# Kernel tuning notes

Measured on AMD Instinct MI355X. Metric: run time of the kernel, lower is better.

Reference implementation:

```python
import jax, jax.numpy as jnp
import numpy as np

N, L, G = 8192, 120, 256          # sentences, seq_len, bags
V, P = 80000, 202                 # word vocab, position vocab
WDIM, FDIM = 50, 5                # word_size, feature_size (width = 50+2*5 = 60)
D, C = 230, 53                    # cnn_layers, num_classes


def setup_inputs() -> dict:
    key = jax.random.key(0)
    ks = jax.random.split(key, 9)
    x = jax.random.randint(ks[0], (N, L), 0, V, dtype=jnp.int32)
    ldist = jax.random.randint(ks[1], (N, L), 0, P, dtype=jnp.int32)
    rdist = jax.random.randint(ks[2], (N, L), 0, P, dtype=jnp.int32)
    # cumulative bag boundaries: 256 equal bags of 32 sentences
    total_shape = (jnp.arange(G + 1, dtype=jnp.int32) * (N // G))
    Wv = jax.random.normal(ks[3], (V, WDIM), dtype=jnp.float32) * 0.1
    pf1 = jax.random.normal(ks[4], (P, FDIM), dtype=jnp.float32) * 0.1
    pf2 = jax.random.normal(ks[5], (P, FDIM), dtype=jnp.float32) * 0.1
    Wc = jax.random.normal(ks[6], (D, 1, 3, WDIM + 2 * FDIM), dtype=jnp.float32) * 0.05
    bc = jnp.zeros((D,), dtype=jnp.float32)
    Wr = jax.random.normal(ks[7], (C, D), dtype=jnp.float32) * 0.05
    br = jnp.zeros((C,), dtype=jnp.float32)
    return dict(x=x, ldist=ldist, rdist=rdist, total_shape=total_shape,
                Wv=Wv, pf1=pf1, pf2=pf2, Wc=Wc, bc=bc, Wr=Wr, br=br)


def reference(x, ldist, rdist, total_shape, Wv, pf1, pf2, Wc, bc, Wr, br):
    n = x.shape[0]
    g = total_shape.shape[0] - 1
    # getEmbeddings: concat word + two position embeddings -> (N, L, 60)
    emb = jnp.concatenate([Wv[x], pf1[ldist], pf2[rdist]], axis=-1)
    # Conv2d(1, D, (3, 60)), VALID -> (N, D, L-2, 1)
    conv = jax.lax.conv_general_dilated(
        emb[:, None, :, :], Wc, window_strides=(1, 1), padding='VALID',
        dimension_numbers=('NCHW', 'OIHW', 'NCHW')) + bc[None, :, None, None]
    # max over positions, squeeze; dropout is identity at eval; tanh
    sent = jnp.tanh(jnp.max(conv, axis=2)[:, :, 0])           # (N, D)
    e = sent @ Wr.T + br                                       # (N, C) batch_e
    # ragged per-bag softmax over sentences (per class), honoring total_shape
    seg = jnp.searchsorted(total_shape, jnp.arange(n), side='right') - 1  # (N,)
    m = jax.ops.segment_max(e, seg, num_segments=g)            # (G, C)
    ex = jnp.exp(e - m[seg])
    den = jax.ops.segment_sum(ex, seg, num_segments=g)
    alpha = ex / den[seg]                                      # (N, C)
    # bag_rep[g, c, :] = sum_i alpha[i, c] * sent[i, :]
    bag = jax.ops.segment_sum(alpha[:, :, None] * sent[:, None, :], seg,
                              num_segments=g)                  # (G, C, D)
    scores = jnp.einsum('gcd,kd->gck', bag, Wr) + br           # (G, C, C)
    probs = jax.nn.softmax(scores, axis=-1)
    return jnp.diagonal(probs, axis1=1, axis2=2)               # (G, C)
```

## Files before the change

kernel.cpp:

```cpp
#include <hip/hip_runtime.h>
#include <hip/hip_bf16.h>

typedef __bf16 bf16x8 __attribute__((ext_vector_type(8)));
typedef float f32x16 __attribute__((ext_vector_type(16)));
typedef unsigned short ushort_t;

#define NSENT 8192
#define LSEQ  120
#define GBAGS 256
#define WDIM_ 50
#define DFILT 230
#define NCLS  53
#define KSTEPS 12
#define BFRAG_ELEMS (24*256*8)

static __device__ __forceinline__ ushort_t f2bf(float f) {
    unsigned int u = __float_as_uint(f);
    unsigned int lsb = (u >> 16) & 1u;
    u += 0x7fffu + lsb;
    return (ushort_t)(u >> 16);
}

__global__ __launch_bounds__(256) void pcnn_prep_b(const float* __restrict__ Wc,
                                                   ushort_t* __restrict__ Bfrag) {
    int idx = blockIdx.x * 256 + threadIdx.x;
    if (idx >= BFRAG_ELEMS) return;
    int c   = idx >> 11;
    int rem = idx & 2047;
    int d   = rem >> 3;
    int j   = rem & 7;
    int k   = c * 8 + j;
    int dh  = k >> 6;
    int w   = k & 63;
    float val = (d < DFILT && w < 60) ? Wc[(d * 3 + dh) * 60 + w] : 0.0f;
    Bfrag[idx] = f2bf(val);
}

#define LROWS 130
__global__ __launch_bounds__(256) void pcnn_conv_sent(
    const int* __restrict__ x, const int* __restrict__ ld, const int* __restrict__ rd,
    const float* __restrict__ Wv, const float* __restrict__ pf1, const float* __restrict__ pf2,
    const ushort_t* __restrict__ Bfrag, const float* __restrict__ bc,
    float* __restrict__ sent) {

    __shared__ __align__(16) unsigned char semb[LROWS * 128];

    const int n    = blockIdx.x;
    const int tid  = threadIdx.x;
    const int wv   = tid >> 6;
    const int lane = tid & 63;
    const int lhalf = lane >> 5;
    const int l31   = lane & 31;

    bf16x8 Bf[2][KSTEPS];
    #pragma unroll
    for (int i = 0; i < 2; ++i) {
        int dcol = (wv * 2 + i) * 32 + l31;
        #pragma unroll
        for (int ks = 0; ks < KSTEPS; ++ks) {
            int c = ks * 2 + lhalf;
            Bf[i][ks] = *reinterpret_cast<const bf16x8*>(Bfrag + ((c * 256 + dcol) << 3));
        }
    }

    if (tid < 80) {
        reinterpret_cast<uint4*>(semb + 120 * 128)[tid] = uint4{0, 0, 0, 0};
    }
    if (tid < 240) {
        int l = tid >> 1, h = tid & 1;
        int tok = x[n * LSEQ + l];
        float v[32];
        const float* wr = Wv + tok * WDIM_;
        if (h == 0) {
            #pragma unroll
            for (int j = 0; j < 16; ++j) {
                float2 t2 = *reinterpret_cast<const float2*>(wr + 2 * j);
                v[2 * j] = t2.x; v[2 * j + 1] = t2.y;
            }
        } else {
            #pragma unroll
            for (int j = 0; j < 9; ++j) {
                float2 t2 = *reinterpret_cast<const float2*>(wr + 32 + 2 * j);
                v[2 * j] = t2.x; v[2 * j + 1] = t2.y;
            }
            int lp = ld[n * LSEQ + l], rp = rd[n * LSEQ + l];
            #pragma unroll
            for (int j = 0; j < 5; ++j) v[18 + j] = pf1[lp * 5 + j];
            #pragma unroll
            for (int j = 0; j < 5; ++j) v[23 + j] = pf2[rp * 5 + j];
            v[28] = v[29] = v[30] = v[31] = 0.0f;
        }
        #pragma unroll
        for (int ch = 0; ch < 4; ++ch) {
            ushort_t u8[8];
            #pragma unroll
            for (int j = 0; j < 8; ++j) u8[j] = f2bf(v[ch * 8 + j]);
            int w0 = h * 32 + ch * 8;
            int byteoff = l * 128 + ((w0 * 2) ^ ((l & 7) << 4));
            *reinterpret_cast<uint4*>(semb + byteoff) = *reinterpret_cast<const uint4*>(u8);
        }
    }
    __syncthreads();

    float dmax0 = -1e30f, dmax1 = -1e30f;
    #pragma unroll
    for (int tt = 0; tt < 4; ++tt) {
        bf16x8 Af[KSTEPS];
        int trow = tt * 32 + l31;
        #pragma unroll
        for (int ks = 0; ks < KSTEPS; ++ks) {
            int dh = ks >> 2, q = ks & 3;
            int l = trow + dh;
            int w0 = q * 16 + lhalf * 8;
            int byteoff = l * 128 + ((w0 * 2) ^ ((l & 7) << 4));
            Af[ks] = *reinterpret_cast<const bf16x8*>(semb + byteoff);
        }
        #pragma unroll
        for (int i = 0; i < 2; ++i) {
            f32x16 acc;
            #pragma unroll
            for (int r = 0; r < 16; ++r) acc[r] = 0.0f;
            #pragma unroll
            for (int ks = 0; ks < KSTEPS; ++ks)
                acc = __builtin_amdgcn_mfma_f32_32x32x16_bf16(Af[ks], Bf[i][ks], acc, 0, 0, 0);
            float m = -1e30f;
            #pragma unroll
            for (int r = 0; r < 16; ++r) {
                int t = tt * 32 + (r & 3) + 8 * (r >> 2) + 4 * lhalf;
                if (t < LSEQ - 2) m = fmaxf(m, acc[r]);
            }
            if (i == 0) dmax0 = fmaxf(dmax0, m);
            else        dmax1 = fmaxf(dmax1, m);
        }
    }
    dmax0 = fmaxf(dmax0, __shfl_xor(dmax0, 32));
    dmax1 = fmaxf(dmax1, __shfl_xor(dmax1, 32));
    if (lhalf == 0) {
        int d0 = (wv * 2 + 0) * 32 + l31;
        int d1 = (wv * 2 + 1) * 32 + l31;
        if (d0 < DFILT) sent[n * DFILT + d0] = tanhf(dmax0 + bc[d0]);
        if (d1 < DFILT) sent[n * DFILT + d1] = tanhf(dmax1 + bc[d1]);
    }
}

#define MAXNS 32
__global__ __launch_bounds__(256) void pcnn_bag(
    const float* __restrict__ sent, const float* __restrict__ Wr, const float* __restrict__ br,
    const int* __restrict__ tshape, float* __restrict__ out) {

    __shared__ float s_sent[MAXNS * DFILT];
    __shared__ float s_e[MAXNS * NCLS];
    __shared__ float s_alpha[MAXNS * NCLS];
    __shared__ float s_sc[NCLS * NCLS];

    const int g = blockIdx.x;
    const int tid = threadIdx.x;
    int start = tshape[g], end = tshape[g + 1];
    int ns = end - start;
    if (ns > MAXNS) ns = MAXNS;

    for (int idx = tid; idx < ns * DFILT; idx += 256)
        s_sent[idx] = sent[start * DFILT + idx];
    __syncthreads();

    for (int task = tid; task < ns * NCLS; task += 256) {
        int i = task / NCLS, c = task - i * NCLS;
        const float* sp = s_sent + i * DFILT;
        const float* wp = Wr + c * DFILT;
        float acc = 0.0f;
        for (int d = 0; d < DFILT; ++d) acc = fmaf(sp[d], wp[d], acc);
        s_e[task] = acc + br[c];
    }
    __syncthreads();

    if (tid < NCLS) {
        int c = tid;
        float m = -1e30f;
        for (int i = 0; i < ns; ++i) m = fmaxf(m, s_e[i * NCLS + c]);
        float den = 0.0f;
        for (int i = 0; i < ns; ++i) {
            float ex = expf(s_e[i * NCLS + c] - m);
            s_alpha[i * NCLS + c] = ex;
            den += ex;
        }
        float inv = 1.0f / den;
        for (int i = 0; i < ns; ++i) s_alpha[i * NCLS + c] *= inv;
    }
    __syncthreads();

    for (int task = tid; task < NCLS * NCLS; task += 256) {
        int c = task / NCLS, k = task - (task / NCLS) * NCLS;
        float brk = br[k];
        float acc = 0.0f;
        for (int i = 0; i < ns; ++i)
            acc = fmaf(s_alpha[i * NCLS + c], s_e[i * NCLS + k] - brk, acc);
        s_sc[task] = acc + brk;
    }
    __syncthreads();

    if (tid < NCLS) {
        int c = tid;
        float m = -1e30f;
        for (int k = 0; k < NCLS; ++k) m = fmaxf(m, s_sc[c * NCLS + k]);
        float den = 0.0f;
        for (int k = 0; k < NCLS; ++k) den += expf(s_sc[c * NCLS + k] - m);
        out[g * NCLS + c] = expf(s_sc[c * NCLS + c] - m) / den;
    }
}

extern "C" void kernel_launch(void* const* d_in, const int* in_sizes, int n_in,
                              void* d_out, int out_size, void* d_ws, size_t ws_size,
                              hipStream_t stream) {
    const int*   x   = (const int*)d_in[0];
    const int*   ldi = (const int*)d_in[1];
    const int*   rdi = (const int*)d_in[2];
    const int*   ts  = (const int*)d_in[3];
    const float* Wv  = (const float*)d_in[4];
    const float* pf1 = (const float*)d_in[5];
    const float* pf2 = (const float*)d_in[6];
    const float* Wc  = (const float*)d_in[7];
    const float* bc  = (const float*)d_in[8];
    const float* Wr  = (const float*)d_in[9];
    const float* br  = (const float*)d_in[10];
    float* out = (float*)d_out;

    ushort_t* Bfrag = (ushort_t*)d_ws;
    float* sent = (float*)((char*)d_ws + BFRAG_ELEMS * sizeof(ushort_t));

    pcnn_prep_b<<<(BFRAG_ELEMS + 255) / 256, 256, 0, stream>>>(Wc, Bfrag);
    pcnn_conv_sent<<<NSENT, 256, 0, stream>>>(x, ldi, rdi, Wv, pf1, pf2, Bfrag, bc, sent);
    pcnn_bag<<<GBAGS, 256, 0, stream>>>(sent, Wr, br, ts, out);
}
```

Baseline: 163.5 us.

## Process four sentences per block with double-buffered gather/MFMA overlap; tile bag kernel

The conv kernel now handles four sentences per block, loading the B fragments once and ping-ponging two LDS embedding buffers so the gather of the next sentence overlaps the MFMA work on the current one. The MFMA loop interleaves the two accumulators per A fragment instead of keeping all twelve A fragments live. The bag kernel stages Wr in LDS, register-tiles the e = sent·Wr^T product 2x4 per thread and pads the class stride. In exchange the grid has fewer blocks (2048), which lowers block-level parallelism, and LDS use per block rises.

```diff
diff --git a/kernel.cpp b/kernel.cpp
--- a/kernel.cpp
+++ b/kernel.cpp
@@ -13,6 +13,8 @@
 #define NCLS  53
 #define KSTEPS 12
 #define BFRAG_ELEMS (24*256*8)
+#define LROWS 130
+#define SPB 4
 
 static __device__ __forceinline__ ushort_t f2bf(float f) {
     unsigned int u = __float_as_uint(f);
@@ -36,76 +38,54 @@
     Bfrag[idx] = f2bf(val);
 }
 
-#define LROWS 130
-__global__ __launch_bounds__(256) void pcnn_conv_sent(
+__device__ __forceinline__ void conv_gather(unsigned char* __restrict__ buf, int n,
     const int* __restrict__ x, const int* __restrict__ ld, const int* __restrict__ rd,
     const float* __restrict__ Wv, const float* __restrict__ pf1, const float* __restrict__ pf2,
-    const ushort_t* __restrict__ Bfrag, const float* __restrict__ bc,
-    float* __restrict__ sent) {
-
-    __shared__ __align__(16) unsigned char semb[LROWS * 128];
-
-    const int n    = blockIdx.x;
-    const int tid  = threadIdx.x;
-    const int wv   = tid >> 6;
-    const int lane = tid & 63;
-    const int lhalf = lane >> 5;
-    const int l31   = lane & 31;
-
-    bf16x8 Bf[2][KSTEPS];
+    int tid) {
+    if (tid >= 240) return;
+    int l = tid >> 1, h = tid & 1;
+    int tok = x[n * LSEQ + l];
+    float v[32];
+    const float* wr = Wv + tok * WDIM_;
+    if (h == 0) {
+        #pragma unroll
+        for (int j = 0; j < 16; ++j) {
+            float2 t2 = *reinterpret_cast<const float2*>(wr + 2 * j);
+            v[2 * j] = t2.x; v[2 * j + 1] = t2.y;
+        }
+    } else {
+        #pragma unroll
+        for (int j = 0; j < 9; ++j) {
+            float2 t2 = *reinterpret_cast<const float2*>(wr + 32 + 2 * j);
+            v[2 * j] = t2.x; v[2 * j + 1] = t2.y;
+        }
+        int lp = ld[n * LSEQ + l], rp = rd[n * LSEQ + l];
+        #pragma unroll
+        for (int j = 0; j < 5; ++j) v[18 + j] = pf1[lp * 5 + j];
+        #pragma unroll
+        for (int j = 0; j < 5; ++j) v[23 + j] = pf2[rp * 5 + j];
+        v[28] = v[29] = v[30] = v[31] = 0.0f;
+    }
     #pragma unroll
-    for (int i = 0; i < 2; ++i) {
-        int dcol = (wv * 2 + i) * 32 + l31;
-        #pragma unroll
-        for (int ks = 0; ks < KSTEPS; ++ks) {
-            int c = ks * 2 + lhalf;
-            Bf[i][ks] = *reinterpret_cast<const bf16x8*>(Bfrag + ((c * 256 + dcol) << 3));
-        }
-    }
-
-    if (tid < 80) {
-        reinterpret_cast<uint4*>(semb + 120 * 128)[tid] = uint4{0, 0, 0, 0};
-    }
-    if (tid < 240) {
-        int l = tid >> 1, h = tid & 1;
-        int tok = x[n * LSEQ + l];
-        float v[32];
-        const float* wr = Wv + tok * WDIM_;
-        if (h == 0) {
-            #pragma unroll
-            for (int j = 0; j < 16; ++j) {
-                float2 t2 = *reinterpret_cast<const float2*>(wr + 2 * j);
-                v[2 * j] = t2.x; v[2 * j + 1] = t2.y;
-            }
-        } else {
-            #pragma unroll
-            for (int j = 0; j < 9; ++j) {
-                float2 t2 = *reinterpret_cast<const float2*>(wr + 32 + 2 * j);
-                v[2 * j] = t2.x; v[2 * j + 1] = t2.y;
-            }
-            int lp = ld[n * LSEQ + l], rp = rd[n * LSEQ + l];
-            #pragma unroll
-            for (int j = 0; j < 5; ++j) v[18 + j] = pf1[lp * 5 + j];
-            #pragma unroll
-            for (int j = 0; j < 5; ++j) v[23 + j] = pf2[rp * 5 + j];
-            v[28] = v[29] = v[30] = v[31] = 0.0f;
-        }
-        #pragma unroll
-        for (int ch = 0; ch < 4; ++ch) {
-            ushort_t u8[8];
-            #pragma unroll
-            for (int j = 0; j < 8; ++j) u8[j] = f2bf(v[ch * 8 + j]);
-            int w0 = h * 32 + ch * 8;
-            int byteoff = l * 128 + ((w0 * 2) ^ ((l & 7) << 4));
-            *reinterpret_cast<uint4*>(semb + byteoff) = *reinterpret_cast<const uint4*>(u8);
-        }
-    }
-    __syncthreads();
-
+    for (int ch = 0; ch < 4; ++ch) {
+        ushort_t u8[8];
+        #pragma unroll
+        for (int j = 0; j < 8; ++j) u8[j] = f2bf(v[ch * 8 + j]);
+        int w0 = h * 32 + ch * 8;
+        int byteoff = l * 128 + ((w0 * 2) ^ ((l & 7) << 4));
+        *reinterpret_cast<uint4*>(buf + byteoff) = *reinterpret_cast<const uint4*>(u8);
+    }
+}
+
+__device__ __forceinline__ void conv_compute(const unsigned char* __restrict__ buf, int n,
+    const bf16x8 (&Bf)[2][KSTEPS], const float* __restrict__ bc, float* __restrict__ sent,
+    int wv, int lhalf, int l31) {
     float dmax0 = -1e30f, dmax1 = -1e30f;
     #pragma unroll
     for (int tt = 0; tt < 4; ++tt) {
-        bf16x8 Af[KSTEPS];
+        f32x16 acc0, acc1;
+        #pragma unroll
+        for (int r = 0; r < 16; ++r) { acc0[r] = 0.0f; acc1[r] = 0.0f; }
         int trow = tt * 32 + l31;
         #pragma unroll
         for (int ks = 0; ks < KSTEPS; ++ks) {
@@ -113,24 +93,15 @@
             int l = trow + dh;
             int w0 = q * 16 + lhalf * 8;
             int byteoff = l * 128 + ((w0 * 2) ^ ((l & 7) << 4));
-            Af[ks] = *reinterpret_cast<const bf16x8*>(semb + byteoff);
-        }
-        #pragma unroll
-        for (int i = 0; i < 2; ++i) {
-            f32x16 acc;
-            #pragma unroll
-            for (int r = 0; r < 16; ++r) acc[r] = 0.0f;
-            #pragma unroll
-            for (int ks = 0; ks < KSTEPS; ++ks)
-                acc = __builtin_amdgcn_mfma_f32_32x32x16_bf16(Af[ks], Bf[i][ks], acc, 0, 0, 0);
-            float m = -1e30f;
-            #pragma unroll
-            for (int r = 0; r < 16; ++r) {
-                int t = tt * 32 + (r & 3) + 8 * (r >> 2) + 4 * lhalf;
-                if (t < LSEQ - 2) m = fmaxf(m, acc[r]);
-            }
-            if (i == 0) dmax0 = fmaxf(dmax0, m);
-            else        dmax1 = fmaxf(dmax1, m);
+            bf16x8 Af = *reinterpret_cast<const bf16x8*>(buf + byteoff);
+            acc0 = __builtin_amdgcn_mfma_f32_32x32x16_bf16(Af, Bf[0][ks], acc0, 0, 0, 0);
+            acc1 = __builtin_amdgcn_mfma_f32_32x32x16_bf16(Af, Bf[1][ks], acc1, 0, 0, 0);
+        }
+        #pragma unroll
+        for (int r = 0; r < 16; ++r) {
+            int t = tt * 32 + (r & 3) + 8 * (r >> 2) + 4 * lhalf;
+            bool valid = (tt < 3) || (t < LSEQ - 2);
+            if (valid) { dmax0 = fmaxf(dmax0, acc0[r]); dmax1 = fmaxf(dmax1, acc1[r]); }
         }
     }
     dmax0 = fmaxf(dmax0, __shfl_xor(dmax0, 32));
@@ -143,15 +114,65 @@
     }
 }
 
+__global__ __launch_bounds__(256) void pcnn_conv_sent(
+    const int* __restrict__ x, const int* __restrict__ ld, const int* __restrict__ rd,
+    const float* __restrict__ Wv, const float* __restrict__ pf1, const float* __restrict__ pf2,
+    const ushort_t* __restrict__ Bfrag, const float* __restrict__ bc,
+    float* __restrict__ sent) {
+
+    __shared__ __align__(16) unsigned char sembA[LROWS * 128];
+    __shared__ __align__(16) unsigned char sembB[LROWS * 128];
+
+    const int n0   = blockIdx.x * SPB;
+    const int tid  = threadIdx.x;
+    const int wv   = tid >> 6;
+    const int lane = tid & 63;
+    const int lhalf = lane >> 5;
+    const int l31   = lane & 31;
+
+    bf16x8 Bf[2][KSTEPS];
+    #pragma unroll
+    for (int i = 0; i < 2; ++i) {
+        int dcol = (wv * 2 + i) * 32 + l31;
+        #pragma unroll
+        for (int ks = 0; ks < KSTEPS; ++ks) {
+            int c = ks * 2 + lhalf;
+            Bf[i][ks] = *reinterpret_cast<const bf16x8*>(Bfrag + ((c * 256 + dcol) << 3));
+        }
+    }
+
+    if (tid < 160) {
+        int b = tid / 80, j = tid % 80;
+        unsigned char* base = (b == 0 ? sembA : sembB) + 120 * 128;
+        reinterpret_cast<uint4*>(base)[j] = uint4{0, 0, 0, 0};
+    }
+    conv_gather(sembA, n0 + 0, x, ld, rd, Wv, pf1, pf2, tid);
+    __syncthreads();
+
+    conv_gather(sembB, n0 + 1, x, ld, rd, Wv, pf1, pf2, tid);
+    conv_compute(sembA, n0 + 0, Bf, bc, sent, wv, lhalf, l31);
+    __syncthreads();
+    conv_gather(sembA, n0 + 2, x, ld, rd, Wv, pf1, pf2, tid);
+    conv_compute(sembB, n0 + 1, Bf, bc, sent, wv, lhalf, l31);
+    __syncthreads();
+    conv_gather(sembB, n0 + 3, x, ld, rd, Wv, pf1, pf2, tid);
+    conv_compute(sembA, n0 + 2, Bf, bc, sent, wv, lhalf, l31);
+    __syncthreads();
+    conv_compute(sembB, n0 + 3, Bf, bc, sent, wv, lhalf, l31);
+}
+
 #define MAXNS 32
+#define CPAD 56
 __global__ __launch_bounds__(256) void pcnn_bag(
     const float* __restrict__ sent, const float* __restrict__ Wr, const float* __restrict__ br,
     const int* __restrict__ tshape, float* __restrict__ out) {
 
     __shared__ float s_sent[MAXNS * DFILT];
-    __shared__ float s_e[MAXNS * NCLS];
-    __shared__ float s_alpha[MAXNS * NCLS];
+    __shared__ float s_Wr[NCLS * DFILT];
+    __shared__ float s_e[MAXNS * CPAD];
+    __shared__ float s_alpha[MAXNS * CPAD];
     __shared__ float s_sc[NCLS * NCLS];
+    __shared__ float s_br[CPAD];
 
     const int g = blockIdx.x;
     const int tid = threadIdx.x;
@@ -159,42 +180,80 @@
     int ns = end - start;
     if (ns > MAXNS) ns = MAXNS;
 
-    for (int idx = tid; idx < ns * DFILT; idx += 256)
-        s_sent[idx] = sent[start * DFILT + idx];
-    __syncthreads();
-
-    for (int task = tid; task < ns * NCLS; task += 256) {
-        int i = task / NCLS, c = task - i * NCLS;
-        const float* sp = s_sent + i * DFILT;
-        const float* wp = Wr + c * DFILT;
-        float acc = 0.0f;
-        for (int d = 0; d < DFILT; ++d) acc = fmaf(sp[d], wp[d], acc);
-        s_e[task] = acc + br[c];
+    {
+        int n2 = ns * (DFILT / 2);
+        const float2* src = reinterpret_cast<const float2*>(sent + start * DFILT);
+        for (int idx = tid; idx < n2; idx += 256)
+            reinterpret_cast<float2*>(s_sent)[idx] = src[idx];
+        const float2* wsrc = reinterpret_cast<const float2*>(Wr);
+        for (int idx = tid; idx < (NCLS * DFILT) / 2; idx += 256)
+            reinterpret_cast<float2*>(s_Wr)[idx] = wsrc[idx];
+        if (tid < NCLS) s_br[tid] = br[tid];
+    }
+    __syncthreads();
+
+    if (tid < 224) {
+        int i0 = tid / 14, c0 = tid % 14;
+        float a00 = 0, a01 = 0, a02 = 0, a03 = 0;
+        float a10 = 0, a11 = 0, a12 = 0, a13 = 0;
+        const float* s0p = s_sent + (2 * i0) * DFILT;
+        const float* s1p = s_sent + (2 * i0 + 1) * DFILT;
+        const float* w0p = s_Wr + (4 * c0 + 0) * DFILT;
+        const float* w1p = s_Wr + (4 * c0 + 1) * DFILT;
+        const float* w2p = (4 * c0 + 2 < NCLS) ? s_Wr + (4 * c0 + 2) * DFILT : s_Wr;
+        const float* w3p = (4 * c0 + 3 < NCLS) ? s_Wr + (4 * c0 + 3) * DFILT : s_Wr;
+        for (int d = 0; d < DFILT; ++d) {
+            float s0 = s0p[d], s1 = s1p[d];
+            float w0 = w0p[d], w1 = w1p[d], w2 = w2p[d], w3 = w3p[d];
+            a00 = fmaf(s0, w0, a00); a01 = fmaf(s0, w1, a01);
+            a02 = fmaf(s0, w2, a02); a03 = fmaf(s0, w3, a03);
+            a10 = fmaf(s1, w0, a10); a11 = fmaf(s1, w1, a11);
+            a12 = fmaf(s1, w2, a12); a13 = fmaf(s1, w3, a13);
+        }
+        float av[2][4] = {{a00, a01, a02, a03}, {a10, a11, a12, a13}};
+        #pragma unroll
+        for (int ii = 0; ii < 2; ++ii) {
+            int i = 2 * i0 + ii;
+            #pragma unroll
+            for (int j = 0; j < 4; ++j) {
+                int c = 4 * c0 + j;
+                if (i < ns && c < NCLS) s_e[i * CPAD + c] = av[ii][j] + s_br[c];
+            }
+        }
     }
     __syncthreads();
 
     if (tid < NCLS) {
         int c = tid;
         float m = -1e30f;
-        for (int i = 0; i < ns; ++i) m = fmaxf(m, s_e[i * NCLS + c]);
+        for (int i = 0; i < ns; ++i) m = fmaxf(m, s_e[i * CPAD + c]);
         float den = 0.0f;
         for (int i = 0; i < ns; ++i) {
-            float ex = expf(s_e[i * NCLS + c] - m);
-            s_alpha[i * NCLS + c] = ex;
+            float ex = expf(s_e[i * CPAD + c] - m);
+            s_alpha[i * CPAD + c] = ex;
             den += ex;
         }
         float inv = 1.0f / den;
-        for (int i = 0; i < ns; ++i) s_alpha[i * NCLS + c] *= inv;
-    }
-    __syncthreads();
-
-    for (int task = tid; task < NCLS * NCLS; task += 256) {
-        int c = task / NCLS, k = task - (task / NCLS) * NCLS;
-        float brk = br[k];
-        float acc = 0.0f;
-        for (int i = 0; i < ns; ++i)
-            acc = fmaf(s_alpha[i * NCLS + c], s_e[i * NCLS + k] - brk, acc);
-        s_sc[task] = acc + brk;
+        for (int i = 0; i < ns; ++i) s_alpha[i * CPAD + c] *= inv;
+    }
+    __syncthreads();
+
+    for (int task = tid; task < NCLS * 14; task += 256) {
+        int c = task / 14, k0 = (task % 14) * 4;
+        float b0 = s_br[k0], b1 = (k0+1<NCLS)?s_br[k0+1]:0.f, b2 = (k0+2<NCLS)?s_br[k0+2]:0.f, b3 = (k0+3<NCLS)?s_br[k0+3]:0.f;
+        float a0 = 0, a1 = 0, a2 = 0, a3 = 0;
+        for (int i = 0; i < ns; ++i) {
+            float al = s_alpha[i * CPAD + c];
+            const float* ep = s_e + i * CPAD + k0;
+            a0 = fmaf(al, ep[0] - b0, a0);
+            a1 = fmaf(al, (k0+1<NCLS?ep[1]:0.f) - b1, a1);
+            a2 = fmaf(al, (k0+2<NCLS?ep[2]:0.f) - b2, a2);
+            a3 = fmaf(al, (k0+3<NCLS?ep[3]:0.f) - b3, a3);
+        }
+        if (k0 + 0 < NCLS) s_sc[c * NCLS + k0 + 0] = a0 + b0;
+        if (k0 + 1 < NCLS) s_sc[c * NCLS + k0 + 1] = a1 + b1;
+        if (k0 + 2 < NCLS) s_sc[c * NCLS + k0 + 2] = a2 + b2;
+        if (k0 + 3 < NCLS) s_sc[c * NCLS + k0 + 3] = a3 + b3;
     }
     __syncthreads();
 
@@ -228,6 +287,6 @@
     float* sent = (float*)((char*)d_ws + BFRAG_ELEMS * sizeof(ushort_t));
 
     pcnn_prep_b<<<(BFRAG_ELEMS + 255) / 256, 256, 0, stream>>>(Wc, Bfrag);
-    pcnn_conv_sent<<<NSENT, 256, 0, stream>>>(x, ldi, rdi, Wv, pf1, pf2, Bfrag, bc, sent);
+    pcnn_conv_sent<<<NSENT / SPB, 256, 0, stream>>>(x, ldi, rdi, Wv, pf1, pf2, Bfrag, bc, sent);
     pcnn_bag<<<GBAGS, 256, 0, stream>>>(sent, Wr, br, ts, out);
 }
```

Result: faster. 150.5 us (-7.9%).
